# Kernel optimization log

Hardware: AMD Instinct MI355X
Metric: run time of the kernel (lower is better)

## Reference

```python
import jax, jax.numpy as jnp
import numpy as np

ALPHA = 0.8
GAMMA = 0.01
BIG = 1e8  # finite stand-in for +inf DP borders (avoids inf-inf NaNs in grads)


def softmin3(a, b, c, gamma):
    # soft-min_gamma over three values, elementwise over batch
    z = jnp.stack([a, b, c], axis=0) * (-1.0 / gamma)
    return -gamma * jax.nn.logsumexp(z, axis=0)


def soft_dtw_batch(D, gamma):
    """Soft-DTW values for a batch of cost matrices.
    D: (B, N, N). Returns (B,) soft-DTW(D_b).
    DP: R[i,j] = D[i,j] + softmin(R[i-1,j-1], R[i-1,j], R[i,j-1]).
    Row-wise lax.scan with an inner column scan; batch stays vectorized.
    """
    B, N, _ = D.shape
    # padded previous row, index 0 is the border column; R[0,0]=0
    init_prev = jnp.full((B, N + 1), BIG, dtype=D.dtype).at[:, 0].set(0.0)

    def row_step(prev, d_row):
        # prev: (B, N+1) padded row i-1; d_row: (B, N) costs of row i
        def col_step(left, inp):
            d, diag, up = inp  # each (B,)
            val = d + softmin3(diag, up, left, gamma)
            return val, val
        _, row = jax.lax.scan(
            col_step,
            jnp.full((B,), BIG, dtype=D.dtype),
            (d_row.T, prev[:, :-1].T, prev[:, 1:].T),
        )
        row = row.T  # (B, N)
        new_prev = jnp.concatenate(
            [jnp.full((B, 1), BIG, dtype=D.dtype), row], axis=1)
        return new_prev, None

    last, _ = jax.lax.scan(row_step, init_prev, jnp.swapaxes(D, 0, 1))
    return last[:, -1]  # R[N, N] per batch


def dilate_loss(pred, target, alpha, gamma):
    # pred, target: (B, N, 1) univariate series
    p = pred[..., 0]
    t = target[..., 0]
    # D[b, i, j] = (target_i - pred_j)^2  (rows = target, cols = pred)
    D = (t[:, :, None] - p[:, None, :]) ** 2  # (B, N, N)

    vals = soft_dtw_batch(D, gamma)           # (B,)
    loss_shape = jnp.mean(vals)

    # soft alignment path = d softDTW / d D (analytic backward in the
    # original PathDTWBatch == autodiff of the DP here)
    E = jax.grad(lambda d: jnp.sum(soft_dtw_batch(d, gamma)))(D)  # (B, N, N)
    path = jnp.mean(E, axis=0)                # (N, N)

    N = p.shape[1]
    idx = jnp.arange(1, N + 1, dtype=p.dtype)
    Omega = (idx[:, None] - idx[None, :]) ** 2  # (N, N) temporal distortion
    loss_temporal = jnp.sum(path * Omega) / (N * N)

    return alpha * loss_shape + (1.0 - alpha) * loss_temporal


def setup_inputs() -> dict:
    key = jax.random.key(0)
    k1, k2 = jax.random.split(key)
    B, N = 128, 256
    pred = jax.random.normal(k1, (B, N, 1), dtype=jnp.float32)
    target = jax.random.normal(k2, (B, N, 1), dtype=jnp.float32)
    return {"pred": pred, "target": target}


def reference(pred, target):
    return dilate_loss(pred, target, ALPHA, GAMMA)
```

## Files before the change

### kernel.cpp

```cpp
#include <hip/hip_runtime.h>

#define NN 256
#define BIGF 1e8f

__global__ void zero_out_k(float* out) {
    if (threadIdx.x == 0) out[0] = 0.0f;
}

__global__ __launch_bounds__(256)
void dilate_dp_k(const float* __restrict__ pred, const float* __restrict__ target,
                 float* __restrict__ Rws, float* __restrict__ out) {
    const float GAM  = 0.01f;
    const float INVG = 100.0f;

    __shared__ float sP[NN + 2], sT[NN + 2];
    __shared__ float rb0[NN + 2], rb1[NN + 2], rb2[NN + 2];
    __shared__ float eb0[NN + 2], eb1[NN + 2], eb2[NN + 2];

    const int tid = threadIdx.x;
    const int b   = blockIdx.x;
    const int i   = tid + 1;
    const size_t base = (size_t)b * (NN * NN);

    sP[tid] = pred[b * NN + tid];
    sT[tid] = target[b * NN + tid];
    if (tid < 2) { sP[NN + tid] = 0.0f; sT[NN + tid] = 0.0f; }

    rb0[tid] = BIGF; rb1[tid] = BIGF; rb2[tid] = BIGF;
    if (tid < 2) { rb0[NN + tid] = BIGF; rb1[NN + tid] = BIGF; rb2[NN + tid] = BIGF; }
    __syncthreads();
    if (tid == 0) rb0[0] = 0.0f;
    __syncthreads();

    float* prev2 = rb0;
    float* prev  = rb1;
    float* cur   = rb2;
    int   off  = 0;
    float rNN  = 0.0f;

    for (int s = 2; s <= 2 * NN; ++s) {
        int ilo = s - NN; if (ilo < 1) ilo = 1;
        int ihi = s - 1;  if (ihi > NN) ihi = NN;
        float val = BIGF;
        if (i >= ilo && i <= ihi) {
            int j = s - i;
            float d  = sT[i - 1] - sP[j - 1]; d *= d;
            float dg = prev2[i - 1];
            float up = prev[i - 1];
            float lf = prev[i];
            float m  = fminf(dg, fminf(up, lf));
            float z  = __expf((m - dg) * INVG) + __expf((m - up) * INVG)
                     + __expf((m - lf) * INVG);
            val = d + m - GAM * __logf(z);
            Rws[base + off + (i - ilo)] = val;
        }
        cur[i] = val;
        if (tid == 0) cur[0] = BIGF;
        if (i == NN && s == 2 * NN) rNN = val;
        off += ihi - ilo + 1;
        __syncthreads();
        float* t0 = prev2; prev2 = prev; prev = cur; cur = t0;
    }

    rb0[tid] = -BIGF; rb1[tid] = -BIGF; rb2[tid] = -BIGF;
    eb0[tid] = 0.0f;  eb1[tid] = 0.0f;  eb2[tid] = 0.0f;
    if (tid < 2) {
        rb0[NN + tid] = -BIGF; rb1[NN + tid] = -BIGF; rb2[NN + tid] = -BIGF;
        eb0[NN + tid] = 0.0f;  eb1[NN + tid] = 0.0f;  eb2[NN + tid] = 0.0f;
    }
    __syncthreads();

    prev2 = rb0; prev = rb1; cur = rb2;
    float* ep2 = eb0; float* ep = eb1; float* ec = eb2;
    float accw = 0.0f;

    for (int s = 2 * NN; s >= 2; --s) {
        int ilo = s - NN; if (ilo < 1) ilo = 1;
        int ihi = s - 1;  if (ihi > NN) ihi = NN;
        off -= ihi - ilo + 1;
        float rv = -BIGF, ev = 0.0f;
        if (i >= ilo && i <= ihi) {
            int j = s - i;
            rv = Rws[base + off + (i - ilo)];
            if (s == 2 * NN) {
                ev = 1.0f;
            } else {
                float rdn = prev[i + 1];
                float rrt = prev[i];
                float rdg = prev2[i + 1];
                float ddn = sT[i]     - sP[j - 1]; ddn *= ddn;
                float drt = sT[i - 1] - sP[j];     drt *= drt;
                float ddg = sT[i]     - sP[j];     ddg *= ddg;
                ev = __expf((rdn - rv - ddn) * INVG) * ep[i + 1]
                   + __expf((rrt - rv - drt) * INVG) * ep[i]
                   + __expf((rdg - rv - ddg) * INVG) * ep2[i + 1];
            }
            int dj = i - j;
            accw += ev * (float)(dj * dj);
        }
        cur[i] = rv;
        ec[i]  = ev;
        __syncthreads();
        float* t0 = prev2; prev2 = prev; prev = cur; cur = t0;
        float* t1 = ep2;   ep2   = ep;   ep   = ec;  ec  = t1;
    }

    for (int o = 32; o >= 1; o >>= 1) accw += __shfl_down(accw, o, 64);
    __syncthreads();
    if ((tid & 63) == 0) eb0[tid >> 6] = accw;
    if (i == NN) eb0[8] = rNN;
    __syncthreads();
    if (tid == 0) {
        float s4 = eb0[0] + eb0[1] + eb0[2] + eb0[3];
        const float SH = 0.8f / 128.0f;
        const float TM = 0.2f / (128.0f * 65536.0f);
        atomicAdd(out, SH * eb0[8] + TM * s4);
    }
}

extern "C" void kernel_launch(void* const* d_in, const int* in_sizes, int n_in,
                              void* d_out, int out_size, void* d_ws, size_t ws_size,
                              hipStream_t stream) {
    const float* pred   = (const float*)d_in[0];
    const float* target = (const float*)d_in[1];
    float* out = (float*)d_out;
    float* Rws = (float*)d_ws;

    zero_out_k<<<1, 64, 0, stream>>>(out);
    dilate_dp_k<<<128, 256, 0, stream>>>(pred, target, Rws, out);
}
```

Measured before the change: 388.1 us.

## Run soft-DTW anti-diagonal DP in a single wavefront with register rows

Replaces the 256-thread block, which needed a __syncthreads per anti-diagonal, with one 64-lane wavefront per batch item. Each lane owns four consecutive rows held in registers, and neighbour values move between lanes with shuffles instead of through shared-memory row buffers. The backward pass prefetches the next diagonal's stored R values one step ahead. This removes block barriers and LDS traffic on the serial critical path, at the cost of four times more serial work per lane and only 64 threads per CU.

After: 602.2 us. +55.2%, slower.

```diff
diff --git a/kernel.cpp b/kernel.cpp
--- a/kernel.cpp
+++ b/kernel.cpp
@@ -2,119 +2,169 @@
 
 #define NN 256
 #define BIGF 1e8f
+#define GAMF 0.01f
+#define INVG 100.0f
 
 __global__ void zero_out_k(float* out) {
     if (threadIdx.x == 0) out[0] = 0.0f;
 }
 
-__global__ __launch_bounds__(256)
-void dilate_dp_k(const float* __restrict__ pred, const float* __restrict__ target,
-                 float* __restrict__ Rws, float* __restrict__ out) {
-    const float GAM  = 0.01f;
-    const float INVG = 100.0f;
+__global__ __launch_bounds__(64)
+void dilate_wave_k(const float* __restrict__ pred, const float* __restrict__ target,
+                   float* __restrict__ Rws, float* __restrict__ out)
+{
+    __shared__ float sP[NN];
+    const int t = threadIdx.x;
+    const int b = blockIdx.x;
+    const size_t base = (size_t)b * (NN * NN);
+    const int r0 = 4 * t;
 
-    __shared__ float sP[NN + 2], sT[NN + 2];
-    __shared__ float rb0[NN + 2], rb1[NN + 2], rb2[NN + 2];
-    __shared__ float eb0[NN + 2], eb1[NN + 2], eb2[NN + 2];
-
-    const int tid = threadIdx.x;
-    const int b   = blockIdx.x;
-    const int i   = tid + 1;
-    const size_t base = (size_t)b * (NN * NN);
-
-    sP[tid] = pred[b * NN + tid];
-    sT[tid] = target[b * NN + tid];
-    if (tid < 2) { sP[NN + tid] = 0.0f; sT[NN + tid] = 0.0f; }
-
-    rb0[tid] = BIGF; rb1[tid] = BIGF; rb2[tid] = BIGF;
-    if (tid < 2) { rb0[NN + tid] = BIGF; rb1[NN + tid] = BIGF; rb2[NN + tid] = BIGF; }
-    __syncthreads();
-    if (tid == 0) rb0[0] = 0.0f;
+    #pragma unroll
+    for (int k = 0; k < 4; ++k) sP[r0 + k] = pred[b * NN + r0 + k];
     __syncthreads();
 
-    float* prev2 = rb0;
-    float* prev  = rb1;
-    float* cur   = rb2;
-    int   off  = 0;
-    float rNN  = 0.0f;
+    float tT[4];
+    #pragma unroll
+    for (int k = 0; k < 4; ++k) tT[k] = target[b * NN + r0 + k];
+    float tTx = target[b * NN + ((r0 + 4 < NN) ? (r0 + 4) : (NN - 1))];
 
+    float rp[4], rpp[4];
+    #pragma unroll
+    for (int k = 0; k < 4; ++k) { rp[k] = BIGF; rpp[k] = BIGF; }
+
+    float pw[4] = {0.f, 0.f, 0.f, 0.f};
+    int ip0 = 0 - r0;
+    float pnext = (ip0 >= 0 && ip0 < NN) ? sP[ip0] : 0.0f;
+
+    int off = 0;
     for (int s = 2; s <= 2 * NN; ++s) {
-        int ilo = s - NN; if (ilo < 1) ilo = 1;
-        int ihi = s - 1;  if (ihi > NN) ihi = NN;
-        float val = BIGF;
-        if (i >= ilo && i <= ihi) {
+        pw[3] = pw[2]; pw[2] = pw[1]; pw[1] = pw[0]; pw[0] = pnext;
+        int ipn = s - 1 - r0;
+        pnext = (ipn >= 0 && ipn < NN) ? sP[ipn] : 0.0f;
+
+        float upS = __shfl_up(rp[3], 1, 64);
+        float dgS = __shfl_up(rpp[3], 1, 64);
+        if (t == 0) { upS = BIGF; dgS = (s == 2) ? 0.0f : BIGF; }
+
+        const int ilo = (s - NN > 1) ? (s - NN) : 1;
+        float rc[4];
+        #pragma unroll
+        for (int k = 0; k < 4; ++k) {
+            int i = r0 + 1 + k;
             int j = s - i;
-            float d  = sT[i - 1] - sP[j - 1]; d *= d;
-            float dg = prev2[i - 1];
-            float up = prev[i - 1];
-            float lf = prev[i];
-            float m  = fminf(dg, fminf(up, lf));
-            float z  = __expf((m - dg) * INVG) + __expf((m - up) * INVG)
-                     + __expf((m - lf) * INVG);
-            val = d + m - GAM * __logf(z);
-            Rws[base + off + (i - ilo)] = val;
+            float dg = (k == 0) ? dgS : rpp[k - 1];
+            float up = (k == 0) ? upS : rp[k - 1];
+            float lf = rp[k];
+            float diff = tT[k] - pw[k];
+            float d = diff * diff;
+            float m = fminf(dg, fminf(up, lf));
+            float z = __expf((m - dg) * INVG) + __expf((m - up) * INVG)
+                    + __expf((m - lf) * INVG);
+            float val = d + m - GAMF * __logf(z);
+            bool act = (j >= 1) && (j <= NN);
+            val = act ? val : BIGF;
+            if (act) Rws[base + off + (i - ilo)] = val;
+            rc[k] = val;
         }
-        cur[i] = val;
-        if (tid == 0) cur[0] = BIGF;
-        if (i == NN && s == 2 * NN) rNN = val;
+        #pragma unroll
+        for (int k = 0; k < 4; ++k) { rpp[k] = rp[k]; rp[k] = rc[k]; }
+        const int ihi = (s - 1 < NN) ? (s - 1) : NN;
         off += ihi - ilo + 1;
-        __syncthreads();
-        float* t0 = prev2; prev2 = prev; prev = cur; cur = t0;
+    }
+    float rNN = rp[3];
+
+    float Rp[4], Rpp[4], Ep[4], Epp[4];
+    #pragma unroll
+    for (int k = 0; k < 4; ++k) { Rp[k] = -BIGF; Rpp[k] = -BIGF; Ep[k] = 0.f; Epp[k] = 0.f; }
+
+    float qw[5];
+    #pragma unroll
+    for (int m = 0; m < 5; ++m) {
+        int id = 2 * NN - 1 - r0 - m;
+        qw[m] = (id >= 0 && id < NN) ? sP[id] : 0.0f;
     }
 
-    rb0[tid] = -BIGF; rb1[tid] = -BIGF; rb2[tid] = -BIGF;
-    eb0[tid] = 0.0f;  eb1[tid] = 0.0f;  eb2[tid] = 0.0f;
-    if (tid < 2) {
-        rb0[NN + tid] = -BIGF; rb1[NN + tid] = -BIGF; rb2[NN + tid] = -BIGF;
-        eb0[NN + tid] = 0.0f;  eb1[NN + tid] = 0.0f;  eb2[NN + tid] = 0.0f;
-    }
-    __syncthreads();
-
-    prev2 = rb0; prev = rb1; cur = rb2;
-    float* ep2 = eb0; float* ep = eb1; float* ec = eb2;
-    float accw = 0.0f;
-
-    for (int s = 2 * NN; s >= 2; --s) {
-        int ilo = s - NN; if (ilo < 1) ilo = 1;
-        int ihi = s - 1;  if (ihi > NN) ihi = NN;
-        off -= ihi - ilo + 1;
-        float rv = -BIGF, ev = 0.0f;
-        if (i >= ilo && i <= ihi) {
-            int j = s - i;
-            rv = Rws[base + off + (i - ilo)];
-            if (s == 2 * NN) {
-                ev = 1.0f;
-            } else {
-                float rdn = prev[i + 1];
-                float rrt = prev[i];
-                float rdg = prev2[i + 1];
-                float ddn = sT[i]     - sP[j - 1]; ddn *= ddn;
-                float drt = sT[i - 1] - sP[j];     drt *= drt;
-                float ddg = sT[i]     - sP[j];     ddg *= ddg;
-                ev = __expf((rdn - rv - ddn) * INVG) * ep[i + 1]
-                   + __expf((rrt - rv - drt) * INVG) * ep[i]
-                   + __expf((rdg - rv - ddg) * INVG) * ep2[i + 1];
-            }
-            int dj = i - j;
-            accw += ev * (float)(dj * dj);
+    float rvp[4];
+    int offb = NN * NN;
+    {
+        int s = 2 * NN;
+        int ilo = (s - NN > 1) ? (s - NN) : 1;
+        int ihi = (s - 1 < NN) ? (s - 1) : NN;
+        offb -= ihi - ilo + 1;
+        #pragma unroll
+        for (int k = 0; k < 4; ++k) {
+            int i = r0 + 1 + k, j = s - i;
+            rvp[k] = -BIGF;
+            if (j >= 1 && j <= NN) rvp[k] = Rws[base + offb + (i - ilo)];
         }
-        cur[i] = rv;
-        ec[i]  = ev;
-        __syncthreads();
-        float* t0 = prev2; prev2 = prev; prev = cur; cur = t0;
-        float* t1 = ep2;   ep2   = ep;   ep   = ec;  ec  = t1;
     }
 
-    for (int o = 32; o >= 1; o >>= 1) accw += __shfl_down(accw, o, 64);
-    __syncthreads();
-    if ((tid & 63) == 0) eb0[tid >> 6] = accw;
-    if (i == NN) eb0[8] = rNN;
-    __syncthreads();
-    if (tid == 0) {
-        float s4 = eb0[0] + eb0[1] + eb0[2] + eb0[3];
+    float acc = 0.0f;
+    for (int s = 2 * NN; s >= 2; --s) {
+        float rv[4];
+        #pragma unroll
+        for (int k = 0; k < 4; ++k) rv[k] = rvp[k];
+
+        if (s > 2) {
+            int sm = s - 1;
+            int ilo_m = (sm - NN > 1) ? (sm - NN) : 1;
+            int ihi_m = (sm - 1 < NN) ? (sm - 1) : NN;
+            offb -= ihi_m - ilo_m + 1;
+            #pragma unroll
+            for (int k = 0; k < 4; ++k) {
+                int i = r0 + 1 + k, j = sm - i;
+                rvp[k] = -BIGF;
+                if (j >= 1 && j <= NN) rvp[k] = Rws[base + offb + (i - ilo_m)];
+            }
+        }
+
+        int iq = s - 6 - r0;
+        float qnext = (iq >= 0 && iq < NN) ? sP[iq] : 0.0f;
+
+        float RdS = __shfl_down(Rp[0], 1, 64);
+        float RgS = __shfl_down(Rpp[0], 1, 64);
+        float EdS = __shfl_down(Ep[0], 1, 64);
+        float EgS = __shfl_down(Epp[0], 1, 64);
+        if (t == 63) { RdS = -BIGF; RgS = -BIGF; EdS = 0.0f; EgS = 0.0f; }
+
+        float Rc[4], Ec[4];
+        #pragma unroll
+        for (int k = 0; k < 4; ++k) {
+            int i = r0 + 1 + k;
+            int j = s - i;
+            bool act = (j >= 1) && (j <= NN);
+            float rvk = rv[k];
+            float rdn = (k < 3) ? Rp[k + 1]  : RdS;
+            float rrt = Rp[k];
+            float rdg = (k < 3) ? Rpp[k + 1] : RgS;
+            float edn = (k < 3) ? Ep[k + 1]  : EdS;
+            float ert = Ep[k];
+            float edg = (k < 3) ? Epp[k + 1] : EgS;
+            float tE = (k < 3) ? tT[k + 1] : tTx;
+            float d1 = tE    - qw[k + 1]; d1 *= d1;
+            float d2 = tT[k] - qw[k];     d2 *= d2;
+            float d3 = tE    - qw[k];     d3 *= d3;
+            float ev = __expf((rdn - rvk - d1) * INVG) * edn
+                     + __expf((rrt - rvk - d2) * INVG) * ert
+                     + __expf((rdg - rvk - d3) * INVG) * edg;
+            if (s == 2 * NN && k == 3 && t == 63) ev = 1.0f;
+            if (!act) { rvk = -BIGF; ev = 0.0f; }
+            float dj = (float)(i - j);
+            acc += ev * dj * dj;
+            Rc[k] = rvk; Ec[k] = ev;
+        }
+        #pragma unroll
+        for (int k = 0; k < 4; ++k) { Rpp[k] = Rp[k]; Rp[k] = Rc[k]; Epp[k] = Ep[k]; Ep[k] = Ec[k]; }
+        qw[0] = qw[1]; qw[1] = qw[2]; qw[2] = qw[3]; qw[3] = qw[4]; qw[4] = qnext;
+    }
+
+    #pragma unroll
+    for (int o = 32; o >= 1; o >>= 1) acc += __shfl_down(acc, o, 64);
+    float rN = __shfl(rNN, 63, 64);
+    if (t == 0) {
         const float SH = 0.8f / 128.0f;
         const float TM = 0.2f / (128.0f * 65536.0f);
-        atomicAdd(out, SH * eb0[8] + TM * s4);
+        atomicAdd(out, SH * rN + TM * acc);
     }
 }
 
@@ -127,5 +177,5 @@
     float* Rws = (float*)d_ws;
 
     zero_out_k<<<1, 64, 0, stream>>>(out);
-    dilate_dp_k<<<128, 256, 0, stream>>>(pred, target, Rws, out);
+    dilate_wave_k<<<128, 64, 0, stream>>>(pred, target, Rws, out);
 }
```
